# Optimization experiments

Hardware: AMD Instinct MI355X
Metric: run time of the kernel (lower is better)

Reference implementation:

```python
import jax, jax.numpy as jnp
import numpy as np

B, S, E = 2, 2048, 2048
NH, NKV, HD = 32, 8, 64
GS = NH // NKV  # group size = 4
EPS = 1e-6
ROPE_THETA = 10000.0


def setup_inputs() -> dict:
    key = jax.random.key(0)
    ks = jax.random.split(key, 6)
    x = jax.random.normal(ks[0], (B, S, E), jnp.float32)
    position_ids = jnp.broadcast_to(jnp.arange(S, dtype=jnp.int32), (B, S))
    # causal additive mask [1,1,S,S]
    causal = jnp.tril(jnp.ones((S, S), jnp.bool_))
    attn_mask = jnp.where(causal, 0.0, -1e9).astype(jnp.float32)[None, None]
    sc = 0.02
    Wq = jax.random.normal(ks[1], (E, NH * HD), jnp.float32) * sc
    Wk = jax.random.normal(ks[2], (E, NKV * HD), jnp.float32) * sc
    Wv = jax.random.normal(ks[3], (E, NKV * HD), jnp.float32) * sc
    Wo = jax.random.normal(ks[4], (NH * HD, E), jnp.float32) * sc
    q_norm_w = jnp.ones((HD,), jnp.float32)
    k_norm_w = jnp.ones((HD,), jnp.float32)
    return {"x": x, "position_ids": position_ids, "attn_mask": attn_mask,
            "Wq": Wq, "Wk": Wk, "Wv": Wv, "Wo": Wo,
            "q_norm_w": q_norm_w, "k_norm_w": k_norm_w}


def rms_norm(x, w):
    dt = x.dtype
    xf = x.astype(jnp.float32)
    xf = xf * jax.lax.rsqrt(jnp.mean(xf * xf, axis=-1, keepdims=True) + EPS)
    return w * xf.astype(dt)


def apply_rope(x, position_ids):
    # x: [B, H, S, D]; rotate-half RoPE
    D = x.shape[-1]
    inv_freq = 1.0 / (ROPE_THETA ** (jnp.arange(0, D, 2, dtype=jnp.float32) / D))
    freqs = position_ids.astype(jnp.float32)[:, :, None] * inv_freq  # [B,S,D/2]
    cos = jnp.cos(freqs)[:, None]  # [B,1,S,D/2]
    sin = jnp.sin(freqs)[:, None]
    x1, x2 = x[..., : D // 2], x[..., D // 2 :]
    return jnp.concatenate([x1 * cos - x2 * sin, x2 * cos + x1 * sin], axis=-1).astype(x.dtype)


def reference(x, position_ids, attn_mask, Wq, Wk, Wv, Wo, q_norm_w, k_norm_w):
    b, s, _ = x.shape
    Q = (x @ Wq).reshape(b, s, NH, HD).transpose(0, 2, 1, 3)   # [B,NH,S,D]
    K = (x @ Wk).reshape(b, s, NKV, HD).transpose(0, 2, 1, 3)  # [B,NKV,S,D]
    V = (x @ Wv).reshape(b, s, NKV, HD).transpose(0, 2, 1, 3)
    Q = rms_norm(Q, q_norm_w)
    K = rms_norm(K, k_norm_w)
    Q = apply_rope(Q, position_ids)
    K = apply_rope(K, position_ids)
    new_kv_cache = (K, V)
    # GQA: head h attends with kv group h // GS == reshape heads -> (NKV, GS)
    Qg = Q.reshape(b, NKV, GS, s, HD)
    scores = jnp.einsum('bgqsd,bgtd->bgqst', Qg, K) / np.float32(np.sqrt(HD))
    scores = scores + attn_mask[:, :, None]  # broadcast over group dim
    attn = jax.nn.softmax(scores.astype(jnp.float32), axis=-1).astype(x.dtype)
    ctx = jnp.einsum('bgqst,bgtd->bgqsd', attn, V)             # [B,NKV,GS,S,D]
    ctx = ctx.reshape(b, NH, s, HD).transpose(0, 2, 1, 3).reshape(b, s, NH * HD)
    output = ctx @ Wo
    return output, new_kv_cache
```

## Files before the change

kernel.cpp:

```cpp
#include <hip/hip_runtime.h>
#include <stdint.h>

#define S_LEN 2048
#define EMB 2048
#define NHEADS 32
#define NKVH 8
#define HDIM 64

typedef float f32x4 __attribute__((ext_vector_type(4)));
typedef float f32x16 __attribute__((ext_vector_type(16)));
typedef __bf16 bf16x8 __attribute__((ext_vector_type(8)));
typedef unsigned int u32x4 __attribute__((ext_vector_type(4)));

typedef const __attribute__((address_space(1))) void* as1cv;
typedef __attribute__((address_space(3))) void* as3v;

__device__ __forceinline__ void gload_lds16(const void* g, void* l) {
  as1cv gp = (as1cv)(uintptr_t)g;
  as3v lp = (as3v)(uintptr_t)l;
  __builtin_amdgcn_global_load_lds(gp, lp, 16, 0, 0);
}

__device__ __forceinline__ unsigned cvt_pk_bf16(float lo, float hi) {
  unsigned r;
// ... 71 lines not shown
  const int NT = K >> 6;
  const int nt = N / BN;
  const int nwg = (M / BM) * nt;
  const int q8 = nwg >> 3;
  int wg = blockIdx.x;
  int swz = (wg & 7) * q8 + (wg >> 3);
  int bm = swz / nt, bn = swz % nt;
  size_t m0 = (size_t)bm * BM, n0 = (size_t)bn * BN;

  int tid = threadIdx.x;
  int L = tid & 63, w = tid >> 6;
  int wrow = w >> 1, wcol = w & 1;
  int l15 = L & 15, hi2 = L >> 4;
  int lx = (l15 & 7) << 4;
  const int cx0 = (hi2 << 4) ^ lx;
  const int cx1 = (64 + (hi2 << 4)) ^ lx;

  int srow = tid >> 3;
  int scol = ((tid & 7) ^ (srow & 7)) << 3;
  const __bf16* pA = A + (size_t)(m0 + srow) * K + scol;
  const __bf16* pB = B + (size_t)(n0 + srow) * K + scol;

  char* smb = (char*)sm;
  const int aRow = (wrow * (BM / 2) + l15) * 128;
  const int bRow = (BM + wcol * (BN / 2) + l15) * 128;

  f32x4 acc[MF][NF];
#pragma unroll
  for (int m = 0; m < MF; ++m)
#pragma unroll
    for (int n = 0; n < NF; ++n) acc[m][n] = (f32x4){0.f, 0.f, 0.f, 0.f};

  auto STG = [&](int buf, int c, int t) {
    const __bf16* s = (c < CHA) ? pA + (size_t)(c << 5) * K + ((size_t)t << 6)
                                : pB + (size_t)((c - CHA) << 5) * K + ((size_t)t << 6);
    gload_lds16(s, smb + buf * (ROWS * 128) + c * 4096 + tid * 16);
  };

#pragma unroll
  for (int c = 0; c < NCALL; ++c) STG(0, c, 0);
#pragma unroll
  for (int c = 0; c < NCALL; ++c) STG(1, c, 1);
  if constexpr (NCALL == 10) asm volatile("s_waitcnt vmcnt(10)" ::: "memory");
  else asm volatile("s_waitcnt vmcnt(8)" ::: "memory");
  __builtin_amdgcn_s_barrier();

  for (int t = 0; t < NT; ++t) {
    const char* aC = smb + (t & 1) * (ROWS * 128);
    bf16x8 af[MF][2], bf[NF][2];
#pragma unroll
    for (int n = 0; n < NF; ++n) {
      bf[n][0] = *(const bf16x8*)(aC + bRow + n * 2048 + cx0);
      bf[n][1] = *(const bf16x8*)(aC + bRow + n * 2048 + cx1);
    }
#pragma unroll
    for (int m = 0; m < MF; ++m) {
      af[m][0] = *(const bf16x8*)(aC + aRow + m * 2048 + cx0);
      af[m][1] = *(const bf16x8*)(aC + aRow + m * 2048 + cx1);
    }
    asm volatile("s_waitcnt lgkmcnt(4)" ::: "memory");
    __builtin_amdgcn_sched_barrier(0);
    __builtin_amdgcn_s_setprio(1);
#pragma unroll
    for (int m = 0; m < MF / 2; ++m)
#pragma unroll
      for (int n = 0; n < NF; ++n)
#pragma unroll
        for (int kk = 0; kk < 2; ++kk)
          acc[m][n] = __builtin_amdgcn_mfma_f32_16x16x32_bf16(
              kk ? af[m][1] : af[m][0], kk ? bf[n][1] : bf[n][0], acc[m][n], 0, 0, 0);
    __builtin_amdgcn_s_setprio(0);
    asm volatile("s_waitcnt lgkmcnt(0)" ::: "memory");
    __builtin_amdgcn_sched_barrier(0);
    __builtin_amdgcn_s_barrier();
    if (t + 2 < NT) {
#pragma unroll
      for (int c = 0; c < NCALL; ++c) STG(t & 1, c, t + 2);
    }
    __builtin_amdgcn_s_setprio(1);
#pragma unroll
    for (int m = MF / 2; m < MF; ++m)
#pragma unroll
      for (int n = 0; n < NF; ++n)
#pragma unroll
        for (int kk = 0; kk < 2; ++kk)
          acc[m][n] = __builtin_amdgcn_mfma_f32_16x16x32_bf16(
              kk ? af[m][1] : af[m][0], kk ? bf[n][1] : bf[n][0], acc[m][n], 0, 0, 0);
    __builtin_amdgcn_s_setprio(0);
    if (t + 2 < NT) {
      if constexpr (NCALL == 10) asm volatile("s_waitcnt vmcnt(10)" ::: "memory");
      else asm volatile("s_waitcnt vmcnt(8)" ::: "memory");
    } else if (t + 1 < NT) {
      asm volatile("s_waitcnt vmcnt(0)" ::: "memory");
    }
    __builtin_amdgcn_s_barrier();
  }

#pragma unroll
  for (int m = 0; m < MF; ++m)
#pragma unroll
    for (int n = 0; n < NF; ++n)
#pragma unroll
      for (int r = 0; r < 4; ++r)
        C[(m0 + wrow * (BM / 2) + m * 16 + (hi2 << 2) + r) * (size_t)N + n0 +
          wcol * (BN / 2) + n * 16 + l15] = (OUT)acc[m][n][r];
}

__global__ __launch_bounds__(256) void rmsrope_kernel(
    const __bf16* __restrict__ QKV, const int* __restrict__ pos,
    const float* __restrict__ qw, const float* __restrict__ kw,
    const float* __restrict__ cosT, const float* __restrict__ sinT,
    __bf16* __restrict__ Qatt, __bf16* __restrict__ Katt, __bf16* __restrict__ Vtatt,
    float* __restrict__ Kc, float* __restrict__ Vc) {
  int token = blockIdx.x;
  int b = token >> 11, s = token & 2047;
  int tid = threadIdx.x, lane = tid & 63, wid = tid >> 6;
  int p = pos[token];
  int i = lane & 31;
  float cs = cosT[p * 32 + i], sn = sinT[p * 32 + i];
  const __bf16* base = QKV + (size_t)token * 3072;
  float qwl = qw[lane], kwl = kw[lane];
  const float qscale = 0.18033688011112042f;

  for (int h = wid; h < NHEADS; h += 4) {
    float v = (float)base[h * 64 + lane];
    float ss = v * v;
#pragma unroll
    for (int m = 1; m < 64; m <<= 1) ss += __shfl_xor(ss, m);
    float xn = v * rsqrtf(ss * (1.0f / 64.0f) + 1e-6f) * qwl;
    float other = __shfl_xor(xn, 32);
    float o = xn * cs + ((lane < 32) ? -other * sn : other * sn);
    Qatt[((size_t)(b * NHEADS + h) * S_LEN + s) * HDIM + lane] = (__bf16)(o * qscale);
  }
  for (int g = wid; g < NKVH; g += 4) {
    float v = (float)base[2048 + g * 64 + lane];
    float ss = v * v;
#pragma unroll
    for (int m = 1; m < 64; m <<= 1) ss += __shfl_xor(ss, m);
    float xn = v * rsqrtf(ss * (1.0f / 64.0f) + 1e-6f) * kwl;
    float other = __shfl_xor(xn, 32);
    float o = xn * cs + ((lane < 32) ? -other * sn : other * sn);
    size_t kidx = ((size_t)(b * NKVH + g) * S_LEN + s) * HDIM + lane;
    Katt[kidx] = (__bf16)o;
    Kc[kidx] = o;
  }
  for (int g = wid; g < NKVH; g += 4) {
    float v = (float)base[2560 + g * 64 + lane];
    size_t vidx = ((size_t)(b * NKVH + g) * S_LEN + s) * HDIM + lane;
    Vc[vidx] = v;
    Vtatt[((size_t)(b * NKVH + g) * HDIM + lane) * S_LEN + s] = (__bf16)v;
  }
}

__global__ __launch_bounds__(256, 2) void attn_kernel(const __bf16* __restrict__ Qatt,
                                                      const __bf16* __restrict__ Katt,
                                                      const __bf16* __restrict__ Vtatt,
                                                      __bf16* __restrict__ ctx) {
  __shared__ __align__(16) __bf16 Ks[2][4096];
  __shared__ __align__(16) __bf16 Vs[2][4096];
  int bid = blockIdx.x;
  int qt, bg;
  if (bid < 256) { qt = 31 - (bid >> 4); bg = bid & 15; }
  else { qt = (bid - 256) >> 4; bg = bid & 15; }
  int b = bg >> 3, g = bg & 7;
  int tid = threadIdx.x, lane = tid & 63, w = tid >> 6;
  int l31 = lane & 31, hi = lane >> 5;
  int h = g * 4 + w;

  const __bf16* Kg = Katt + (size_t)bg * (S_LEN * HDIM);
  const __bf16* Vg = Vtatt + (size_t)bg * (HDIM * S_LEN);
  const __bf16* Qg = Qatt + ((size_t)(b * NHEADS + h) * S_LEN + qt * 64 + l31) * HDIM;

  bf16x8 qf0[4], qf1[4];
#pragma unroll
  for (int ds = 0; ds < 4; ++ds) {
    qf0[ds] = *(const bf16x8*)(Qg + ds * 16 + (hi << 3));
    qf1[ds] = *(const bf16x8*)(Qg + 32 * HDIM + ds * 16 + (hi << 3));
  }

  f32x16 acc00, acc01, acc10, acc11;
#pragma unroll
  for (int r = 0; r < 16; ++r) { acc00[r] = 0.f; acc01[r] = 0.f; acc10[r] = 0.f; acc11[r] = 0.f; }
  float l0 = 0.f, l1 = 0.f;

  int sr = tid >> 3;
  int sc = ((tid & 7) ^ (sr & 7)) << 3;
  const __bf16* Ksrc = Kg + (size_t)sr * HDIM + sc;
  const __bf16* Vsrc = Vg + (size_t)sr * S_LEN + sc;

  gload_lds16(Ksrc, &Ks[0][tid * 8]);
  gload_lds16(Ksrc + 32 * HDIM, &Ks[0][2048 + tid * 8]);
  gload_lds16(Vsrc, &Vs[0][tid * 8]);
  gload_lds16(Vsrc + (size_t)32 * S_LEN, &Vs[0][2048 + tid * 8]);
  __syncthreads();

  int rx = (l31 & 7) << 4;

  for (int t = 0; t <= qt; ++t) {
    int cur = t & 1;
    if (t < qt) {
      const __bf16* kn = Ksrc + (size_t)(t + 1) * (64 * HDIM);
      const __bf16* vn = Vsrc + (size_t)(t + 1) * 64;
      gload_lds16(kn, &Ks[cur ^ 1][tid * 8]);
      gload_lds16(kn + 32 * HDIM, &Ks[cur ^ 1][2048 + tid * 8]);
      gload_lds16(vn, &Vs[cur ^ 1][tid * 8]);
      gload_lds16(vn + (size_t)32 * S_LEN, &Vs[cur ^ 1][2048 + tid * 8]);
    }
    f32x16 s00, s01, s10, s11;
#pragma unroll
    for (int r = 0; r < 16; ++r) { s00[r] = 0.f; s01[r] = 0.f; s10[r] = 0.f; s11[r] = 0.f; }
    {
      const char* kb0 = (const char*)Ks[cur] + (size_t)l31 * 128;
      const char* kb1 = kb0 + 4096;
#pragma unroll
      for (int dstep = 0; dstep < 4; ++dstep) {
        int cb = dstep * 32 + (hi << 4);
        bf16x8 k0 = *(const bf16x8*)(kb0 + (cb ^ rx));
        bf16x8 k1 = *(const bf16x8*)(kb1 + (cb ^ rx));
        s00 = __builtin_amdgcn_mfma_f32_32x32x16_bf16(k0, qf0[dstep], s00, 0, 0, 0);
        s01 = __builtin_amdgcn_mfma_f32_32x32x16_bf16(k1, qf0[dstep], s01, 0, 0, 0);
        s10 = __builtin_amdgcn_mfma_f32_32x32x16_bf16(k0, qf1[dstep], s10, 0, 0, 0);
        s11 = __builtin_amdgcn_mfma_f32_32x32x16_bf16(k1, qf1[dstep], s11, 0, 0, 0);
      }
    }
    if (t == qt) {
#pragma unroll
      for (int r = 0; r < 16; ++r) {
        int kb = (r & 3) + 8 * (r >> 2) + (hi << 2);
        if (kb > l31) { s00[r] = -3e38f; s11[r] = -3e38f; }
        s01[r] = -3e38f;
      }
    }
#pragma unroll
    for (int r = 0; r < 16; ++r) {
      s00[r] = __builtin_amdgcn_exp2f(s00[r]);
      s01[r] = __builtin_amdgcn_exp2f(s01[r]);
      s10[r] = __builtin_amdgcn_exp2f(s10[r]);
      s11[r] = __builtin_amdgcn_exp2f(s11[r]);
    }
    {
      float a0 = 0.f, a1 = 0.f, a2 = 0.f, a3 = 0.f;
      float b0 = 0.f, b1 = 0.f, b2 = 0.f, b3 = 0.f;
#pragma unroll
      for (int r = 0; r < 16; r += 4) {
        a0 += s00[r]; a1 += s00[r + 1]; a2 += s00[r + 2]; a3 += s00[r + 3];
        a0 += s01[r]; a1 += s01[r + 1]; a2 += s01[r + 2]; a3 += s01[r + 3];
        b0 += s10[r]; b1 += s10[r + 1]; b2 += s10[r + 2]; b3 += s10[r + 3];
        b0 += s11[r]; b1 += s11[r + 1]; b2 += s11[r + 2]; b3 += s11[r + 3];
      }
      l0 += (a0 + a1) + (a2 + a3);
      l1 += (b0 + b1) + (b2 + b3);
    }
    bf16x8 pf0[4], pf1[4];
    {
      unsigned wd[8];
#pragma unroll
      for (int i = 0; i < 8; ++i) wd[i] = cvt_pk_bf16(s00[2 * i], s00[2 * i + 1]);
      permswap(wd[0], wd[2]); permswap(wd[1], wd[3]);
      permswap(wd[4], wd[6]); permswap(wd[5], wd[7]);
      pf0[0] = pack4(wd[0], wd[1], wd[2], wd[3]);
      pf0[1] = pack4(wd[4], wd[5], wd[6], wd[7]);
#pragma unroll
      for (int i = 0; i < 8; ++i) wd[i] = cvt_pk_bf16(s01[2 * i], s01[2 * i + 1]);
      permswap(wd[0], wd[2]); permswap(wd[1], wd[3]);
      permswap(wd[4], wd[6]); permswap(wd[5], wd[7]);
      pf0[2] = pack4(wd[0], wd[1], wd[2], wd[3]);
      pf0[3] = pack4(wd[4], wd[5], wd[6], wd[7]);
#pragma unroll
      for (int i = 0; i < 8; ++i) wd[i] = cvt_pk_bf16(s10[2 * i], s10[2 * i + 1]);
      permswap(wd[0], wd[2]); permswap(wd[1], wd[3]);
      permswap(wd[4], wd[6]); permswap(wd[5], wd[7]);
      pf1[0] = pack4(wd[0], wd[1], wd[2], wd[3]);
      pf1[1] = pack4(wd[4], wd[5], wd[6], wd[7]);
#pragma unroll
      for (int i = 0; i < 8; ++i) wd[i] = cvt_pk_bf16(s11[2 * i], s11[2 * i + 1]);
      permswap(wd[0], wd[2]); permswap(wd[1], wd[3]);
      permswap(wd[4], wd[6]); permswap(wd[5], wd[7]);
      pf1[2] = pack4(wd[0], wd[1], wd[2], wd[3]);
      pf1[3] = pack4(wd[4], wd[5], wd[6], wd[7]);
    }
    {
      const char* vb0 = (const char*)Vs[cur] + (size_t)l31 * 128;
      const char* vb1 = vb0 + 4096;
#pragma unroll
      for (int ks = 0; ks < 4; ++ks) {
        int cb = ks * 32 + (hi << 4);
        bf16x8 v0 = *(const bf16x8*)(vb0 + (cb ^ rx));
        bf16x8 v1 = *(const bf16x8*)(vb1 + (cb ^ rx));
        acc00 = __builtin_amdgcn_mfma_f32_32x32x16_bf16(v0, pf0[ks], acc00, 0, 0, 0);
        acc01 = __builtin_amdgcn_mfma_f32_32x32x16_bf16(v1, pf0[ks], acc01, 0, 0, 0);
        acc10 = __builtin_amdgcn_mfma_f32_32x32x16_bf16(v0, pf1[ks], acc10, 0, 0, 0);
        acc11 = __builtin_amdgcn_mfma_f32_32x32x16_bf16(v1, pf1[ks], acc11, 0, 0, 0);
      }
    }
    __syncthreads();
  }

  l0 += __shfl_xor(l0, 32);
  l1 += __shfl_xor(l1, 32);
  float inv0 = 1.f / l0, inv1 = 1.f / l1;
  size_t orow0 = ((size_t)(b * S_LEN + qt * 64 + l31)) * EMB + h * HDIM;
  size_t orow1 = orow0 + (size_t)32 * EMB;
#pragma unroll
  for (int r = 0; r < 16; r += 2) {
    int d = (r & 3) + 8 * (r >> 2) + (hi << 2);
    unsigned w00 = cvt_pk_bf16(acc00[r] * inv0, acc00[r + 1] * inv0);
    unsigned w01 = cvt_pk_bf16(acc01[r] * inv0, acc01[r + 1] * inv0);
    unsigned w10 = cvt_pk_bf16(acc10[r] * inv1, acc10[r + 1] * inv1);
    unsigned w11 = cvt_pk_bf16(acc11[r] * inv1, acc11[r + 1] * inv1);
    *(unsigned*)((char*)ctx + (orow0 + d) * 2) = w00;
    *(unsigned*)((char*)ctx + (orow0 + 32 + d) * 2) = w01;
    *(unsigned*)((char*)ctx + (orow1 + d) * 2) = w10;
    *(unsigned*)((char*)ctx + (orow1 + 32 + d) * 2) = w11;
  }
}

extern "C" void kernel_launch(void* const* d_in, const int* in_sizes, int n_in,
                              void* d_out, int out_size, void* d_ws, size_t ws_size,
                              hipStream_t stream) {
  const float* x = (const float*)d_in[0];
  const int* pos = (const int*)d_in[1];
  const float* Wq = (const float*)d_in[3];
  const float* Wk = (const float*)d_in[4];
  const float* Wv = (const float*)d_in[5];
  const float* Wo = (const float*)d_in[6];
  const float* qw = (const float*)d_in[7];
  const float* kw = (const float*)d_in[8];

  float* out = (float*)d_out;
  float* Kc = out + (size_t)2 * 2048 * 2048;
  float* Vc = Kc + (size_t)2 * 8 * 2048 * 64;

  char* ws = (char*)d_ws;
  size_t off = 0;
  auto alloc = [&](size_t bytes) {
    char* p = ws + off;
    off += (bytes + 255) & ~(size_t)255;
    return (void*)p;
  };
  __bf16* xb = (__bf16*)alloc((size_t)4096 * 2048 * 2);
  __bf16* Wcat = (__bf16*)alloc((size_t)3072 * 2048 * 2);
  __bf16* Wot = (__bf16*)alloc((size_t)2048 * 2048 * 2);
  __bf16* QKV = (__bf16*)alloc((size_t)4096 * 3072 * 2);
  __bf16* ctx = (__bf16*)alloc((size_t)4096 * 2048 * 2);
  __bf16* Qatt = (__bf16*)alloc((size_t)2 * 32 * 2048 * 64 * 2);
  __bf16* Katt = (__bf16*)alloc((size_t)2 * 8 * 2048 * 64 * 2);
  __bf16* Vtat = (__bf16*)alloc((size_t)2 * 8 * 2048 * 64 * 2);
  float* cosT = (float*)alloc((size_t)2048 * 32 * 4);
  float* sinT = (float*)alloc((size_t)2048 * 32 * 4);

  rope_table_kernel<<<2048, 64, 0, stream>>>(cosT, sinT);
  cast_bf16_kernel<<<4096, 256, 0, stream>>>(x, xb, 4096 * 2048 / 8);
  transpose_cast_kernel<<<dim3(32, 32), 256, 0, stream>>>(Wq, Wcat, 2048, 2048);
  transpose_cast_kernel<<<dim3(8, 32), 256, 0, stream>>>(Wk, Wcat + (size_t)2048 * 2048, 2048, 512);
  transpose_cast_kernel<<<dim3(8, 32), 256, 0, stream>>>(Wv, Wcat + (size_t)2560 * 2048, 2048, 512);
  transpose_cast_kernel<<<dim3(32, 32), 256, 0, stream>>>(Wo, Wot, 2048, 2048);
  gemm4w_kernel<128, 192, __bf16><<<512, 256, 0, stream>>>(xb, Wcat, QKV, 4096, 3072, 2048);
  rmsrope_kernel<<<4096, 256, 0, stream>>>(QKV, pos, qw, kw, cosT, sinT, Qatt, Katt, Vtat, Kc, Vc);
  attn_kernel<<<512, 256, 0, stream>>>(Qatt, Katt, Vtat, ctx);
  gemm4w_kernel<128, 128, float><<<512, 256, 0, stream>>>(ctx, Wot, out, 4096, 2048, 2048);
}
```

Baseline: 186.2 us.

## Split KV tiles across two wave groups and pair causal q-tiles per block

The attention kernel now runs 512 threads per block. Two groups of four waves each process alternating KV tiles for the same query tile, and their partial accumulators and row sums are combined through LDS at the end. Each block handles both a long causal q-tile (31-x) and a short one (x) in sequence, which balances work across 256 blocks. Loads now stage two KV tiles at once with explicit waitcnt and barriers. This adds an LDS reduction and extra barriers, and drops occupancy to one block per CU in exchange for more in-flight work per query tile.

After: 188.2 us. About the same (+1.1%).

```diff
diff --git a/kernel.cpp b/kernel.cpp
--- a/kernel.cpp
+++ b/kernel.cpp
@@ -247,166 +247,216 @@
   }
 }
 
-__global__ __launch_bounds__(256, 2) void attn_kernel(const __bf16* __restrict__ Qatt,
+__global__ __launch_bounds__(512, 1) void attn_kernel(const __bf16* __restrict__ Qatt,
                                                       const __bf16* __restrict__ Katt,
                                                       const __bf16* __restrict__ Vtatt,
                                                       __bf16* __restrict__ ctx) {
-  __shared__ __align__(16) __bf16 Ks[2][4096];
-  __shared__ __align__(16) __bf16 Vs[2][4096];
+  __shared__ __align__(16) char smem[67584];
   int bid = blockIdx.x;
-  int qt, bg;
-  if (bid < 256) { qt = 31 - (bid >> 4); bg = bid & 15; }
-  else { qt = (bid - 256) >> 4; bg = bid & 15; }
+  int x = bid >> 4;
+  int bg = bid & 15;
   int b = bg >> 3, g = bg & 7;
   int tid = threadIdx.x, lane = tid & 63, w = tid >> 6;
+  int hq = w & 3, par = w >> 2;
+  int h = g * 4 + hq;
   int l31 = lane & 31, hi = lane >> 5;
-  int h = g * 4 + w;
+  int rx = (l31 & 7) << 4;
 
   const __bf16* Kg = Katt + (size_t)bg * (S_LEN * HDIM);
   const __bf16* Vg = Vtatt + (size_t)bg * (HDIM * S_LEN);
-  const __bf16* Qg = Qatt + ((size_t)(b * NHEADS + h) * S_LEN + qt * 64 + l31) * HDIM;
-
-  bf16x8 qf0[4], qf1[4];
-#pragma unroll
-  for (int ds = 0; ds < 4; ++ds) {
-    qf0[ds] = *(const bf16x8*)(Qg + ds * 16 + (hi << 3));
-    qf1[ds] = *(const bf16x8*)(Qg + 32 * HDIM + ds * 16 + (hi << 3));
-  }
-
-  f32x16 acc00, acc01, acc10, acc11;
-#pragma unroll
-  for (int r = 0; r < 16; ++r) { acc00[r] = 0.f; acc01[r] = 0.f; acc10[r] = 0.f; acc11[r] = 0.f; }
-  float l0 = 0.f, l1 = 0.f;
 
   int sr = tid >> 3;
   int sc = ((tid & 7) ^ (sr & 7)) << 3;
   const __bf16* Ksrc = Kg + (size_t)sr * HDIM + sc;
   const __bf16* Vsrc = Vg + (size_t)sr * S_LEN + sc;
 
-  gload_lds16(Ksrc, &Ks[0][tid * 8]);
-  gload_lds16(Ksrc + 32 * HDIM, &Ks[0][2048 + tid * 8]);
-  gload_lds16(Vsrc, &Vs[0][tid * 8]);
-  gload_lds16(Vsrc + (size_t)32 * S_LEN, &Vs[0][2048 + tid * 8]);
-  __syncthreads();
-
-  int rx = (l31 & 7) << 4;
-
-  for (int t = 0; t <= qt; ++t) {
-    int cur = t & 1;
-    if (t < qt) {
-      const __bf16* kn = Ksrc + (size_t)(t + 1) * (64 * HDIM);
-      const __bf16* vn = Vsrc + (size_t)(t + 1) * 64;
-      gload_lds16(kn, &Ks[cur ^ 1][tid * 8]);
-      gload_lds16(kn + 32 * HDIM, &Ks[cur ^ 1][2048 + tid * 8]);
-      gload_lds16(vn, &Vs[cur ^ 1][tid * 8]);
-      gload_lds16(vn + (size_t)32 * S_LEN, &Vs[cur ^ 1][2048 + tid * 8]);
-    }
-    f32x16 s00, s01, s10, s11;
-#pragma unroll
-    for (int r = 0; r < 16; ++r) { s00[r] = 0.f; s01[r] = 0.f; s10[r] = 0.f; s11[r] = 0.f; }
-    {
-      const char* kb0 = (const char*)Ks[cur] + (size_t)l31 * 128;
-      const char* kb1 = kb0 + 4096;
-#pragma unroll
-      for (int dstep = 0; dstep < 4; ++dstep) {
-        int cb = dstep * 32 + (hi << 4);
-        bf16x8 k0 = *(const bf16x8*)(kb0 + (cb ^ rx));
-        bf16x8 k1 = *(const bf16x8*)(kb1 + (cb ^ rx));
-        s00 = __builtin_amdgcn_mfma_f32_32x32x16_bf16(k0, qf0[dstep], s00, 0, 0, 0);
-        s01 = __builtin_amdgcn_mfma_f32_32x32x16_bf16(k1, qf0[dstep], s01, 0, 0, 0);
-        s10 = __builtin_amdgcn_mfma_f32_32x32x16_bf16(k0, qf1[dstep], s10, 0, 0, 0);
-        s11 = __builtin_amdgcn_mfma_f32_32x32x16_bf16(k1, qf1[dstep], s11, 0, 0, 0);
+  float* lm = (float*)(smem + 65536);
+
+  auto STAGE = [&](int pair, int slot, int t) {
+    gload_lds16(Ksrc + (size_t)t * (64 * HDIM), smem + (pair * 2 + slot) * 8192 + tid * 16);
+    gload_lds16(Vsrc + (size_t)t * 64, smem + 32768 + (pair * 2 + slot) * 8192 + tid * 16);
+  };
+
+#pragma unroll 1
+  for (int phase = 0; phase < 2; ++phase) {
+    int qt = phase == 0 ? (31 - x) : x;
+    const __bf16* Qg = Qatt + ((size_t)(b * NHEADS + h) * S_LEN + qt * 64 + l31) * HDIM;
+    bf16x8 qf0[4], qf1[4];
+#pragma unroll
+    for (int ds = 0; ds < 4; ++ds) {
+      qf0[ds] = *(const bf16x8*)(Qg + ds * 16 + (hi << 3));
+      qf1[ds] = *(const bf16x8*)(Qg + 32 * HDIM + ds * 16 + (hi << 3));
+    }
+    f32x16 acc00, acc01, acc10, acc11;
+#pragma unroll
+    for (int r = 0; r < 16; ++r) { acc00[r] = 0.f; acc01[r] = 0.f; acc10[r] = 0.f; acc11[r] = 0.f; }
+    float l0 = 0.f, l1 = 0.f;
+
+    int niter = (qt + 2) >> 1;
+    STAGE(0, 0, 0);
+    STAGE(0, 1, qt > 0 ? 1 : 0);
+
+#pragma unroll 1
+    for (int i = 0; i < niter; ++i) {
+      int pcur = i & 1;
+      int ta = 2 * i + 2;
+      if (ta <= qt) {
+        int tb = (ta + 1 <= qt) ? ta + 1 : qt;
+        STAGE(pcur ^ 1, 0, ta);
+        STAGE(pcur ^ 1, 1, tb);
+        asm volatile("s_waitcnt vmcnt(4)" ::: "memory");
+      } else {
+        asm volatile("s_waitcnt vmcnt(0)" ::: "memory");
       }
-    }
-    if (t == qt) {
-#pragma unroll
-      for (int r = 0; r < 16; ++r) {
-        int kb = (r & 3) + 8 * (r >> 2) + (hi << 2);
-        if (kb > l31) { s00[r] = -3e38f; s11[r] = -3e38f; }
-        s01[r] = -3e38f;
+      __builtin_amdgcn_s_barrier();
+      int t = 2 * i + par;
+      if (t <= qt) {
+        const char* Kt = smem + (pcur * 2 + par) * 8192;
+        const char* Vt = smem + 32768 + (pcur * 2 + par) * 8192;
+        f32x16 s00, s01, s10, s11;
+#pragma unroll
+        for (int r = 0; r < 16; ++r) { s00[r] = 0.f; s01[r] = 0.f; s10[r] = 0.f; s11[r] = 0.f; }
+        {
+          const char* kb0 = Kt + (size_t)l31 * 128;
+          const char* kb1 = kb0 + 4096;
+#pragma unroll
+          for (int dstep = 0; dstep < 4; ++dstep) {
+            int cb = dstep * 32 + (hi << 4);
+            bf16x8 k0 = *(const bf16x8*)(kb0 + (cb ^ rx));
+            bf16x8 k1 = *(const bf16x8*)(kb1 + (cb ^ rx));
+            s00 = __builtin_amdgcn_mfma_f32_32x32x16_bf16(k0, qf0[dstep], s00, 0, 0, 0);
+            s01 = __builtin_amdgcn_mfma_f32_32x32x16_bf16(k1, qf0[dstep], s01, 0, 0, 0);
+            s10 = __builtin_amdgcn_mfma_f32_32x32x16_bf16(k0, qf1[dstep], s10, 0, 0, 0);
+            s11 = __builtin_amdgcn_mfma_f32_32x32x16_bf16(k1, qf1[dstep], s11, 0, 0, 0);
+          }
+        }
+        if (t == qt) {
+#pragma unroll
+          for (int r = 0; r < 16; ++r) {
+            int kb = (r & 3) + 8 * (r >> 2) + (hi << 2);
+            if (kb > l31) { s00[r] = -3e38f; s11[r] = -3e38f; }
+            s01[r] = -3e38f;
+          }
+        }
+#pragma unroll
+        for (int r = 0; r < 16; ++r) {
+          s00[r] = __builtin_amdgcn_exp2f(s00[r]);
+          s01[r] = __builtin_amdgcn_exp2f(s01[r]);
+          s10[r] = __builtin_amdgcn_exp2f(s10[r]);
+          s11[r] = __builtin_amdgcn_exp2f(s11[r]);
+        }
+        {
+          float a0 = 0.f, a1 = 0.f, a2 = 0.f, a3 = 0.f;
+          float b0 = 0.f, b1 = 0.f, b2 = 0.f, b3 = 0.f;
+#pragma unroll
+          for (int r = 0; r < 16; r += 4) {
+            a0 += s00[r]; a1 += s00[r + 1]; a2 += s00[r + 2]; a3 += s00[r + 3];
+            a0 += s01[r]; a1 += s01[r + 1]; a2 += s01[r + 2]; a3 += s01[r + 3];
+            b0 += s10[r]; b1 += s10[r + 1]; b2 += s10[r + 2]; b3 += s10[r + 3];
+            b0 += s11[r]; b1 += s11[r + 1]; b2 += s11[r + 2]; b3 += s11[r + 3];
+          }
+          l0 += (a0 + a1) + (a2 + a3);
+          l1 += (b0 + b1) + (b2 + b3);
+        }
+        bf16x8 pf0[4], pf1[4];
+        {
+          unsigned wd[8];
+#pragma unroll
+          for (int j = 0; j < 8; ++j) wd[j] = cvt_pk_bf16(s00[2 * j], s00[2 * j + 1]);
+          permswap(wd[0], wd[2]); permswap(wd[1], wd[3]);
+          permswap(wd[4], wd[6]); permswap(wd[5], wd[7]);
+          pf0[0] = pack4(wd[0], wd[1], wd[2], wd[3]);
+          pf0[1] = pack4(wd[4], wd[5], wd[6], wd[7]);
+#pragma unroll
+          for (int j = 0; j < 8; ++j) wd[j] = cvt_pk_bf16(s01[2 * j], s01[2 * j + 1]);
+          permswap(wd[0], wd[2]); permswap(wd[1], wd[3]);
+          permswap(wd[4], wd[6]); permswap(wd[5], wd[7]);
+          pf0[2] = pack4(wd[0], wd[1], wd[2], wd[3]);
+          pf0[3] = pack4(wd[4], wd[5], wd[6], wd[7]);
+#pragma unroll
+          for (int j = 0; j < 8; ++j) wd[j] = cvt_pk_bf16(s10[2 * j], s10[2 * j + 1]);
+          permswap(wd[0], wd[2]); permswap(wd[1], wd[3]);
+          permswap(wd[4], wd[6]); permswap(wd[5], wd[7]);
+          pf1[0] = pack4(wd[0], wd[1], wd[2], wd[3]);
+          pf1[1] = pack4(wd[4], wd[5], wd[6], wd[7]);
+#pragma unroll
+          for (int j = 0; j < 8; ++j) wd[j] = cvt_pk_bf16(s11[2 * j], s11[2 * j + 1]);
+          permswap(wd[0], wd[2]); permswap(wd[1], wd[3]);
+          permswap(wd[4], wd[6]); permswap(wd[5], wd[7]);
+          pf1[2] = pack4(wd[0], wd[1], wd[2], wd[3]);
+          pf1[3] = pack4(wd[4], wd[5], wd[6], wd[7]);
+        }
+        {
+          const char* vb0 = Vt + (size_t)l31 * 128;
+          const char* vb1 = vb0 + 4096;
+#pragma unroll
+          for (int ks = 0; ks < 4; ++ks) {
+            int cb = ks * 32 + (hi << 4);
+            bf16x8 v0 = *(const bf16x8*)(vb0 + (cb ^ rx));
+            bf16x8 v1 = *(const bf16x8*)(vb1 + (cb ^ rx));
+            acc00 = __builtin_amdgcn_mfma_f32_32x32x16_bf16(v0, pf0[ks], acc00, 0, 0, 0);
+            acc01 = __builtin_amdgcn_mfma_f32_32x32x16_bf16(v1, pf0[ks], acc01, 0, 0, 0);
+            acc10 = __builtin_amdgcn_mfma_f32_32x32x16_bf16(v0, pf1[ks], acc10, 0, 0, 0);
+            acc11 = __builtin_amdgcn_mfma_f32_32x32x16_bf16(v1, pf1[ks], acc11, 0, 0, 0);
+          }
+        }
       }
-    }
-#pragma unroll
-    for (int r = 0; r < 16; ++r) {
-      s00[r] = __builtin_amdgcn_exp2f(s00[r]);
-      s01[r] = __builtin_amdgcn_exp2f(s01[r]);
-      s10[r] = __builtin_amdgcn_exp2f(s10[r]);
-      s11[r] = __builtin_amdgcn_exp2f(s11[r]);
-    }
-    {
-      float a0 = 0.f, a1 = 0.f, a2 = 0.f, a3 = 0.f;
-      float b0 = 0.f, b1 = 0.f, b2 = 0.f, b3 = 0.f;
-#pragma unroll
-      for (int r = 0; r < 16; r += 4) {
-        a0 += s00[r]; a1 += s00[r + 1]; a2 += s00[r + 2]; a3 += s00[r + 3];
-        a0 += s01[r]; a1 += s01[r + 1]; a2 += s01[r + 2]; a3 += s01[r + 3];
-        b0 += s10[r]; b1 += s10[r + 1]; b2 += s10[r + 2]; b3 += s10[r + 3];
-        b0 += s11[r]; b1 += s11[r + 1]; b2 += s11[r + 2]; b3 += s11[r + 3];
+      asm volatile("s_waitcnt lgkmcnt(0)" ::: "memory");
+      __builtin_amdgcn_sched_barrier(0);
+      __builtin_amdgcn_s_barrier();
+    }
+
+    char* om = smem + hq * 16384 + lane * 16;
+    if (par == 1) {
+#pragma unroll
+      for (int j = 0; j < 4; ++j) {
+        *(f32x4*)(om + j * 1024) = (f32x4){acc00[4 * j], acc00[4 * j + 1], acc00[4 * j + 2], acc00[4 * j + 3]};
+        *(f32x4*)(om + (4 + j) * 1024) = (f32x4){acc01[4 * j], acc01[4 * j + 1], acc01[4 * j + 2], acc01[4 * j + 3]};
+        *(f32x4*)(om + (8 + j) * 1024) = (f32x4){acc10[4 * j], acc10[4 * j + 1], acc10[4 * j + 2], acc10[4 * j + 3]};
+        *(f32x4*)(om + (12 + j) * 1024) = (f32x4){acc11[4 * j], acc11[4 * j + 1], acc11[4 * j + 2], acc11[4 * j + 3]};
       }
-      l0 += (a0 + a1) + (a2 + a3);
-      l1 += (b0 + b1) + (b2 + b3);
-    }
-    bf16x8 pf0[4], pf1[4];
-    {
-      unsigned wd[8];
-#pragma unroll
-      for (int i = 0; i < 8; ++i) wd[i] = cvt_pk_bf16(s00[2 * i], s00[2 * i + 1]);
-      permswap(wd[0], wd[2]); permswap(wd[1], wd[3]);
-      permswap(wd[4], wd[6]); permswap(wd[5], wd[7]);
-      pf0[0] = pack4(wd[0], wd[1], wd[2], wd[3]);
-      pf0[1] = pack4(wd[4], wd[5], wd[6], wd[7]);
-#pragma unroll
-      for (int i = 0; i < 8; ++i) wd[i] = cvt_pk_bf16(s01[2 * i], s01[2 * i + 1]);
-      permswap(wd[0], wd[2]); permswap(wd[1], wd[3]);
-      permswap(wd[4], wd[6]); permswap(wd[5], wd[7]);
-      pf0[2] = pack4(wd[0], wd[1], wd[2], wd[3]);
-      pf0[3] = pack4(wd[4], wd[5], wd[6], wd[7]);
-#pragma unroll
-      for (int i = 0; i < 8; ++i) wd[i] = cvt_pk_bf16(s10[2 * i], s10[2 * i + 1]);
-      permswap(wd[0], wd[2]); permswap(wd[1], wd[3]);
-      permswap(wd[4], wd[6]); permswap(wd[5], wd[7]);
-      pf1[0] = pack4(wd[0], wd[1], wd[2], wd[3]);
-      pf1[1] = pack4(wd[4], wd[5], wd[6], wd[7]);
-#pragma unroll
-      for (int i = 0; i < 8; ++i) wd[i] = cvt_pk_bf16(s11[2 * i], s11[2 * i + 1]);
-      permswap(wd[0], wd[2]); permswap(wd[1], wd[3]);
-      permswap(wd[4], wd[6]); permswap(wd[5], wd[7]);
-      pf1[2] = pack4(wd[0], wd[1], wd[2], wd[3]);
-      pf1[3] = pack4(wd[4], wd[5], wd[6], wd[7]);
-    }
-    {
-      const char* vb0 = (const char*)Vs[cur] + (size_t)l31 * 128;
-      const char* vb1 = vb0 + 4096;
-#pragma unroll
-      for (int ks = 0; ks < 4; ++ks) {
-        int cb = ks * 32 + (hi << 4);
-        bf16x8 v0 = *(const bf16x8*)(vb0 + (cb ^ rx));
-        bf16x8 v1 = *(const bf16x8*)(vb1 + (cb ^ rx));
-        acc00 = __builtin_amdgcn_mfma_f32_32x32x16_bf16(v0, pf0[ks], acc00, 0, 0, 0);
-        acc01 = __builtin_amdgcn_mfma_f32_32x32x16_bf16(v1, pf0[ks], acc01, 0, 0, 0);
-        acc10 = __builtin_amdgcn_mfma_f32_32x32x16_bf16(v0, pf1[ks], acc10, 0, 0, 0);
-        acc11 = __builtin_amdgcn_mfma_f32_32x32x16_bf16(v1, pf1[ks], acc11, 0, 0, 0);
+      lm[hq * 128 + lane] = l0;
+      lm[hq * 128 + 64 + lane] = l1;
+    }
+    asm volatile("s_waitcnt lgkmcnt(0)" ::: "memory");
+    __builtin_amdgcn_s_barrier();
+    if (par == 0) {
+#pragma unroll
+      for (int j = 0; j < 4; ++j) {
+        f32x4 c0 = *(const f32x4*)(om + j * 1024);
+        f32x4 c1 = *(const f32x4*)(om + (4 + j) * 1024);
+        f32x4 c2 = *(const f32x4*)(om + (8 + j) * 1024);
+        f32x4 c3 = *(const f32x4*)(om + (12 + j) * 1024);
+#pragma unroll
+        for (int e = 0; e < 4; ++e) {
+          acc00[4 * j + e] += c0[e];
+          acc01[4 * j + e] += c1[e];
+          acc10[4 * j + e] += c2[e];
+          acc11[4 * j + e] += c3[e];
+        }
       }
-    }
-    __syncthreads();
-  }
-
-  l0 += __shfl_xor(l0, 32);
-  l1 += __shfl_xor(l1, 32);
-  float inv0 = 1.f / l0, inv1 = 1.f / l1;
-  size_t orow0 = ((size_t)(b * S_LEN + qt * 64 + l31)) * EMB + h * HDIM;
-  size_t orow1 = orow0 + (size_t)32 * EMB;
-#pragma unroll
-  for (int r = 0; r < 16; r += 2) {
-    int d = (r & 3) + 8 * (r >> 2) + (hi << 2);
-    unsigned w00 = cvt_pk_bf16(acc00[r] * inv0, acc00[r + 1] * inv0);
-    unsigned w01 = cvt_pk_bf16(acc01[r] * inv0, acc01[r + 1] * inv0);
-    unsigned w10 = cvt_pk_bf16(acc10[r] * inv1, acc10[r + 1] * inv1);
-    unsigned w11 = cvt_pk_bf16(acc11[r] * inv1, acc11[r + 1] * inv1);
-    *(unsigned*)((char*)ctx + (orow0 + d) * 2) = w00;
-    *(unsigned*)((char*)ctx + (orow0 + 32 + d) * 2) = w01;
-    *(unsigned*)((char*)ctx + (orow1 + d) * 2) = w10;
-    *(unsigned*)((char*)ctx + (orow1 + 32 + d) * 2) = w11;
+      l0 += lm[hq * 128 + lane];
+      l1 += lm[hq * 128 + 64 + lane];
+      l0 += __shfl_xor(l0, 32);
+      l1 += __shfl_xor(l1, 32);
+      float inv0 = 1.f / l0, inv1 = 1.f / l1;
+      size_t orow0 = ((size_t)(b * S_LEN + qt * 64 + l31)) * EMB + h * HDIM;
+      size_t orow1 = orow0 + (size_t)32 * EMB;
+#pragma unroll
+      for (int r = 0; r < 16; r += 2) {
+        int d = (r & 3) + 8 * (r >> 2) + (hi << 2);
+        unsigned w00 = cvt_pk_bf16(acc00[r] * inv0, acc00[r + 1] * inv0);
+        unsigned w01 = cvt_pk_bf16(acc01[r] * inv0, acc01[r + 1] * inv0);
+        unsigned w10 = cvt_pk_bf16(acc10[r] * inv1, acc10[r + 1] * inv1);
+        unsigned w11 = cvt_pk_bf16(acc11[r] * inv1, acc11[r + 1] * inv1);
+        *(unsigned*)((char*)ctx + (orow0 + d) * 2) = w00;
+        *(unsigned*)((char*)ctx + (orow0 + 32 + d) * 2) = w01;
+        *(unsigned*)((char*)ctx + (orow1 + d) * 2) = w10;
+        *(unsigned*)((char*)ctx + (orow1 + 32 + d) * 2) = w11;
+      }
+    }
+    asm volatile("s_waitcnt lgkmcnt(0)" ::: "memory");
+    __builtin_amdgcn_s_barrier();
   }
 }
 
@@ -452,6 +502,6 @@
   transpose_cast_kernel<<<dim3(32, 32), 256, 0, stream>>>(Wo, Wot, 2048, 2048);
   gemm4w_kernel<128, 192, __bf16><<<512, 256, 0, stream>>>(xb, Wcat, QKV, 4096, 3072, 2048);
   rmsrope_kernel<<<4096, 256, 0, stream>>>(QKV, pos, qw, kw, cosT, sinT, Qatt, Katt, Vtat, Kc, Vc);
-  attn_kernel<<<512, 256, 0, stream>>>(Qatt, Katt, Vtat, ctx);
+  attn_kernel<<<256, 512, 0, stream>>>(Qatt, Katt, Vtat, ctx);
   gemm4w_kernel<128, 128, float><<<512, 256, 0, stream>>>(ctx, Wot, out, 4096, 2048, 2048);
 }
```

## Pair complementary 32-row query tiles per block with triple-buffered K/V staging

Applied to the files above, without the earlier changes.

The attention kernel now gives each warp 32 query rows instead of 64. Each block processes two complementary causal tiles (j and 63-j) one after the other, so every block does an equal amount of work. K/V tiles are staged through a three-slot LDS ring with explicit vmcnt waits, which lets loads run two tiles ahead, and the MFMA sections are raised with s_setprio. The cost is that each K/V tile loaded into LDS now serves half as many query rows, which raises LDS read traffic per MFMA and adds barrier overhead.

After: 192.6 us. 1.03x slower.

```diff
diff --git a/kernel.cpp b/kernel.cpp
--- a/kernel.cpp
+++ b/kernel.cpp
@@ -251,162 +251,153 @@
                                                       const __bf16* __restrict__ Katt,
                                                       const __bf16* __restrict__ Vtatt,
                                                       __bf16* __restrict__ ctx) {
-  __shared__ __align__(16) __bf16 Ks[2][4096];
-  __shared__ __align__(16) __bf16 Vs[2][4096];
+  __shared__ __align__(16) char smem[49152];
   int bid = blockIdx.x;
-  int qt, bg;
-  if (bid < 256) { qt = 31 - (bid >> 4); bg = bid & 15; }
-  else { qt = (bid - 256) >> 4; bg = bid & 15; }
+  int p = bid >> 4, bg = bid & 15;
   int b = bg >> 3, g = bg & 7;
   int tid = threadIdx.x, lane = tid & 63, w = tid >> 6;
   int l31 = lane & 31, hi = lane >> 5;
   int h = g * 4 + w;
+  int rx = (l31 & 7) << 4;
 
   const __bf16* Kg = Katt + (size_t)bg * (S_LEN * HDIM);
   const __bf16* Vg = Vtatt + (size_t)bg * (HDIM * S_LEN);
-  const __bf16* Qg = Qatt + ((size_t)(b * NHEADS + h) * S_LEN + qt * 64 + l31) * HDIM;
-
-  bf16x8 qf0[4], qf1[4];
-#pragma unroll
-  for (int ds = 0; ds < 4; ++ds) {
-    qf0[ds] = *(const bf16x8*)(Qg + ds * 16 + (hi << 3));
-    qf1[ds] = *(const bf16x8*)(Qg + 32 * HDIM + ds * 16 + (hi << 3));
-  }
-
-  f32x16 acc00, acc01, acc10, acc11;
-#pragma unroll
-  for (int r = 0; r < 16; ++r) { acc00[r] = 0.f; acc01[r] = 0.f; acc10[r] = 0.f; acc11[r] = 0.f; }
-  float l0 = 0.f, l1 = 0.f;
 
   int sr = tid >> 3;
   int sc = ((tid & 7) ^ (sr & 7)) << 3;
   const __bf16* Ksrc = Kg + (size_t)sr * HDIM + sc;
   const __bf16* Vsrc = Vg + (size_t)sr * S_LEN + sc;
 
-  gload_lds16(Ksrc, &Ks[0][tid * 8]);
-  gload_lds16(Ksrc + 32 * HDIM, &Ks[0][2048 + tid * 8]);
-  gload_lds16(Vsrc, &Vs[0][tid * 8]);
-  gload_lds16(Vsrc + (size_t)32 * S_LEN, &Vs[0][2048 + tid * 8]);
-  __syncthreads();
-
-  int rx = (l31 & 7) << 4;
-
-  for (int t = 0; t <= qt; ++t) {
-    int cur = t & 1;
-    if (t < qt) {
-      const __bf16* kn = Ksrc + (size_t)(t + 1) * (64 * HDIM);
-      const __bf16* vn = Vsrc + (size_t)(t + 1) * 64;
-      gload_lds16(kn, &Ks[cur ^ 1][tid * 8]);
-      gload_lds16(kn + 32 * HDIM, &Ks[cur ^ 1][2048 + tid * 8]);
-      gload_lds16(vn, &Vs[cur ^ 1][tid * 8]);
-      gload_lds16(vn + (size_t)32 * S_LEN, &Vs[cur ^ 1][2048 + tid * 8]);
-    }
-    f32x16 s00, s01, s10, s11;
-#pragma unroll
-    for (int r = 0; r < 16; ++r) { s00[r] = 0.f; s01[r] = 0.f; s10[r] = 0.f; s11[r] = 0.f; }
-    {
-      const char* kb0 = (const char*)Ks[cur] + (size_t)l31 * 128;
-      const char* kb1 = kb0 + 4096;
-#pragma unroll
-      for (int dstep = 0; dstep < 4; ++dstep) {
-        int cb = dstep * 32 + (hi << 4);
-        bf16x8 k0 = *(const bf16x8*)(kb0 + (cb ^ rx));
-        bf16x8 k1 = *(const bf16x8*)(kb1 + (cb ^ rx));
-        s00 = __builtin_amdgcn_mfma_f32_32x32x16_bf16(k0, qf0[dstep], s00, 0, 0, 0);
-        s01 = __builtin_amdgcn_mfma_f32_32x32x16_bf16(k1, qf0[dstep], s01, 0, 0, 0);
-        s10 = __builtin_amdgcn_mfma_f32_32x32x16_bf16(k0, qf1[dstep], s10, 0, 0, 0);
-        s11 = __builtin_amdgcn_mfma_f32_32x32x16_bf16(k1, qf1[dstep], s11, 0, 0, 0);
-      }
-    }
-    if (t == qt) {
+  auto STAGE = [&](int slot, int t) {
+    char* base = smem + slot * 16384;
+    const __bf16* kt = Ksrc + (size_t)t * (64 * HDIM);
+    const __bf16* vt = Vsrc + (size_t)t * 64;
+    gload_lds16(kt, base + tid * 16);
+    gload_lds16(kt + 32 * HDIM, base + 4096 + tid * 16);
+    gload_lds16(vt, base + 8192 + tid * 16);
+    gload_lds16(vt + (size_t)32 * S_LEN, base + 12288 + tid * 16);
+  };
+
+#pragma unroll 1
+  for (int phase = 0; phase < 2; ++phase) {
+    int j = phase ? (63 - p) : p;
+    int tl = j >> 1;
+    const __bf16* Qg = Qatt + ((size_t)(b * NHEADS + h) * S_LEN + j * 32 + l31) * HDIM;
+    bf16x8 qf[4];
+#pragma unroll
+    for (int ds = 0; ds < 4; ++ds) qf[ds] = *(const bf16x8*)(Qg + ds * 16 + (hi << 3));
+
+    f32x16 acc0, acc1;
+#pragma unroll
+    for (int r = 0; r < 16; ++r) { acc0[r] = 0.f; acc1[r] = 0.f; }
+    float l_run = 0.f;
+
+    STAGE(0, 0);
+    if (tl >= 1) STAGE(1, 1);
+
+#pragma unroll 1
+    for (int i = 0; i <= tl; ++i) {
+      if (i + 2 <= tl) {
+        STAGE((i + 2) % 3, i + 2);
+        asm volatile("s_waitcnt vmcnt(8)" ::: "memory");
+      } else if (i + 1 <= tl) {
+        asm volatile("s_waitcnt vmcnt(4)" ::: "memory");
+      } else {
+        asm volatile("s_waitcnt vmcnt(0)" ::: "memory");
+      }
+      __builtin_amdgcn_s_barrier();
+
+      const char* Kt = smem + (i % 3) * 16384;
+      const char* Vt = Kt + 8192;
+      f32x16 s0, s1;
+#pragma unroll
+      for (int r = 0; r < 16; ++r) { s0[r] = 0.f; s1[r] = 0.f; }
+      {
+        const char* kb0 = Kt + (size_t)l31 * 128;
+        const char* kb1 = kb0 + 4096;
+        __builtin_amdgcn_s_setprio(1);
+#pragma unroll
+        for (int dstep = 0; dstep < 4; ++dstep) {
+          int cb = dstep * 32 + (hi << 4);
+          bf16x8 k0 = *(const bf16x8*)(kb0 + (cb ^ rx));
+          bf16x8 k1 = *(const bf16x8*)(kb1 + (cb ^ rx));
+          s0 = __builtin_amdgcn_mfma_f32_32x32x16_bf16(k0, qf[dstep], s0, 0, 0, 0);
+          s1 = __builtin_amdgcn_mfma_f32_32x32x16_bf16(k1, qf[dstep], s1, 0, 0, 0);
+        }
+        __builtin_amdgcn_s_setprio(0);
+      }
+      if (i == tl) {
+#pragma unroll
+        for (int r = 0; r < 16; ++r) {
+          int kb = (r & 3) + 8 * (r >> 2) + (hi << 2);
+          if (j & 1) {
+            if (kb > l31) s1[r] = -3e38f;
+          } else {
+            if (kb > l31) s0[r] = -3e38f;
+            s1[r] = -3e38f;
+          }
+        }
+      }
 #pragma unroll
       for (int r = 0; r < 16; ++r) {
-        int kb = (r & 3) + 8 * (r >> 2) + (hi << 2);
-        if (kb > l31) { s00[r] = -3e38f; s11[r] = -3e38f; }
-        s01[r] = -3e38f;
-      }
-    }
-#pragma unroll
-    for (int r = 0; r < 16; ++r) {
-      s00[r] = __builtin_amdgcn_exp2f(s00[r]);
-      s01[r] = __builtin_amdgcn_exp2f(s01[r]);
-      s10[r] = __builtin_amdgcn_exp2f(s10[r]);
-      s11[r] = __builtin_amdgcn_exp2f(s11[r]);
-    }
-    {
-      float a0 = 0.f, a1 = 0.f, a2 = 0.f, a3 = 0.f;
-      float b0 = 0.f, b1 = 0.f, b2 = 0.f, b3 = 0.f;
-#pragma unroll
-      for (int r = 0; r < 16; r += 4) {
-        a0 += s00[r]; a1 += s00[r + 1]; a2 += s00[r + 2]; a3 += s00[r + 3];
-        a0 += s01[r]; a1 += s01[r + 1]; a2 += s01[r + 2]; a3 += s01[r + 3];
-        b0 += s10[r]; b1 += s10[r + 1]; b2 += s10[r + 2]; b3 += s10[r + 3];
-        b0 += s11[r]; b1 += s11[r + 1]; b2 += s11[r + 2]; b3 += s11[r + 3];
-      }
-      l0 += (a0 + a1) + (a2 + a3);
-      l1 += (b0 + b1) + (b2 + b3);
-    }
-    bf16x8 pf0[4], pf1[4];
-    {
-      unsigned wd[8];
-#pragma unroll
-      for (int i = 0; i < 8; ++i) wd[i] = cvt_pk_bf16(s00[2 * i], s00[2 * i + 1]);
-      permswap(wd[0], wd[2]); permswap(wd[1], wd[3]);
-      permswap(wd[4], wd[6]); permswap(wd[5], wd[7]);
-      pf0[0] = pack4(wd[0], wd[1], wd[2], wd[3]);
-      pf0[1] = pack4(wd[4], wd[5], wd[6], wd[7]);
-#pragma unroll
-      for (int i = 0; i < 8; ++i) wd[i] = cvt_pk_bf16(s01[2 * i], s01[2 * i + 1]);
-      permswap(wd[0], wd[2]); permswap(wd[1], wd[3]);
-      permswap(wd[4], wd[6]); permswap(wd[5], wd[7]);
-      pf0[2] = pack4(wd[0], wd[1], wd[2], wd[3]);
-      pf0[3] = pack4(wd[4], wd[5], wd[6], wd[7]);
-#pragma unroll
-      for (int i = 0; i < 8; ++i) wd[i] = cvt_pk_bf16(s10[2 * i], s10[2 * i + 1]);
-      permswap(wd[0], wd[2]); permswap(wd[1], wd[3]);
-      permswap(wd[4], wd[6]); permswap(wd[5], wd[7]);
-      pf1[0] = pack4(wd[0], wd[1], wd[2], wd[3]);
-      pf1[1] = pack4(wd[4], wd[5], wd[6], wd[7]);
-#pragma unroll
-      for (int i = 0; i < 8; ++i) wd[i] = cvt_pk_bf16(s11[2 * i], s11[2 * i + 1]);
-      permswap(wd[0], wd[2]); permswap(wd[1], wd[3]);
-      permswap(wd[4], wd[6]); permswap(wd[5], wd[7]);
-      pf1[2] = pack4(wd[0], wd[1], wd[2], wd[3]);
-      pf1[3] = pack4(wd[4], wd[5], wd[6], wd[7]);
-    }
-    {
-      const char* vb0 = (const char*)Vs[cur] + (size_t)l31 * 128;
-      const char* vb1 = vb0 + 4096;
-#pragma unroll
-      for (int ks = 0; ks < 4; ++ks) {
-        int cb = ks * 32 + (hi << 4);
-        bf16x8 v0 = *(const bf16x8*)(vb0 + (cb ^ rx));
-        bf16x8 v1 = *(const bf16x8*)(vb1 + (cb ^ rx));
-        acc00 = __builtin_amdgcn_mfma_f32_32x32x16_bf16(v0, pf0[ks], acc00, 0, 0, 0);
-        acc01 = __builtin_amdgcn_mfma_f32_32x32x16_bf16(v1, pf0[ks], acc01, 0, 0, 0);
-        acc10 = __builtin_amdgcn_mfma_f32_32x32x16_bf16(v0, pf1[ks], acc10, 0, 0, 0);
-        acc11 = __builtin_amdgcn_mfma_f32_32x32x16_bf16(v1, pf1[ks], acc11, 0, 0, 0);
-      }
-    }
-    __syncthreads();
-  }
-
-  l0 += __shfl_xor(l0, 32);
-  l1 += __shfl_xor(l1, 32);
-  float inv0 = 1.f / l0, inv1 = 1.f / l1;
-  size_t orow0 = ((size_t)(b * S_LEN + qt * 64 + l31)) * EMB + h * HDIM;
-  size_t orow1 = orow0 + (size_t)32 * EMB;
-#pragma unroll
-  for (int r = 0; r < 16; r += 2) {
-    int d = (r & 3) + 8 * (r >> 2) + (hi << 2);
-    unsigned w00 = cvt_pk_bf16(acc00[r] * inv0, acc00[r + 1] * inv0);
-    unsigned w01 = cvt_pk_bf16(acc01[r] * inv0, acc01[r + 1] * inv0);
-    unsigned w10 = cvt_pk_bf16(acc10[r] * inv1, acc10[r + 1] * inv1);
-    unsigned w11 = cvt_pk_bf16(acc11[r] * inv1, acc11[r + 1] * inv1);
-    *(unsigned*)((char*)ctx + (orow0 + d) * 2) = w00;
-    *(unsigned*)((char*)ctx + (orow0 + 32 + d) * 2) = w01;
-    *(unsigned*)((char*)ctx + (orow1 + d) * 2) = w10;
-    *(unsigned*)((char*)ctx + (orow1 + 32 + d) * 2) = w11;
+        s0[r] = __builtin_amdgcn_exp2f(s0[r]);
+        s1[r] = __builtin_amdgcn_exp2f(s1[r]);
+      }
+      {
+        float a0 = 0.f, a1 = 0.f, a2 = 0.f, a3 = 0.f;
+#pragma unroll
+        for (int r = 0; r < 16; r += 4) {
+          a0 += s0[r]; a1 += s0[r + 1]; a2 += s0[r + 2]; a3 += s0[r + 3];
+          a0 += s1[r]; a1 += s1[r + 1]; a2 += s1[r + 2]; a3 += s1[r + 3];
+        }
+        l_run += (a0 + a1) + (a2 + a3);
+      }
+      bf16x8 pf[4];
+      {
+        unsigned wd[8];
+#pragma unroll
+        for (int q = 0; q < 8; ++q) wd[q] = cvt_pk_bf16(s0[2 * q], s0[2 * q + 1]);
+        permswap(wd[0], wd[2]); permswap(wd[1], wd[3]);
+        permswap(wd[4], wd[6]); permswap(wd[5], wd[7]);
+        pf[0] = pack4(wd[0], wd[1], wd[2], wd[3]);
+        pf[1] = pack4(wd[4], wd[5], wd[6], wd[7]);
+#pragma unroll
+        for (int q = 0; q < 8; ++q) wd[q] = cvt_pk_bf16(s1[2 * q], s1[2 * q + 1]);
+        permswap(wd[0], wd[2]); permswap(wd[1], wd[3]);
+        permswap(wd[4], wd[6]); permswap(wd[5], wd[7]);
+        pf[2] = pack4(wd[0], wd[1], wd[2], wd[3]);
+        pf[3] = pack4(wd[4], wd[5], wd[6], wd[7]);
+      }
+      {
+        const char* vb0 = Vt + (size_t)l31 * 128;
+        const char* vb1 = vb0 + 4096;
+        __builtin_amdgcn_s_setprio(1);
+#pragma unroll
+        for (int ks = 0; ks < 4; ++ks) {
+          int cb = ks * 32 + (hi << 4);
+          bf16x8 v0 = *(const bf16x8*)(vb0 + (cb ^ rx));
+          bf16x8 v1 = *(const bf16x8*)(vb1 + (cb ^ rx));
+          acc0 = __builtin_amdgcn_mfma_f32_32x32x16_bf16(v0, pf[ks], acc0, 0, 0, 0);
+          acc1 = __builtin_amdgcn_mfma_f32_32x32x16_bf16(v1, pf[ks], acc1, 0, 0, 0);
+        }
+        __builtin_amdgcn_s_setprio(0);
+      }
+      asm volatile("s_waitcnt lgkmcnt(0)" ::: "memory");
+      __builtin_amdgcn_sched_barrier(0);
+      __builtin_amdgcn_s_barrier();
+    }
+
+    l_run += __shfl_xor(l_run, 32);
+    float inv = 1.f / l_run;
+    size_t orow = ((size_t)(b * S_LEN + j * 32 + l31)) * EMB + h * HDIM;
+#pragma unroll
+    for (int r = 0; r < 16; r += 2) {
+      int d = (r & 3) + 8 * (r >> 2) + (hi << 2);
+      unsigned w0 = cvt_pk_bf16(acc0[r] * inv, acc0[r + 1] * inv);
+      unsigned w1 = cvt_pk_bf16(acc1[r] * inv, acc1[r + 1] * inv);
+      *(unsigned*)((char*)ctx + (orow + d) * 2) = w0;
+      *(unsigned*)((char*)ctx + (orow + 32 + d) * 2) = w1;
+    }
   }
 }
 
```

## Triple-buffer K/V tiles in attention with explicit vmcnt waits and MFMA priority

Applied to the files above, without the earlier changes.

Replaces the double-buffered K/V LDS staging with a three-slot ring that prefetches two tiles ahead. Explicit s_waitcnt vmcnt counts let the kernel wait only for the current tile's loads, with raw s_barrier in place of __syncthreads. The MFMA sections are wrapped in s_setprio to favour matrix issue across waves. LDS use grows from 32KB to 48KB per block, which may limit how many blocks fit per CU, and the hand-set vmcnt values depend on the exact number of outstanding loads.

New measurement: 190.5 us. +2.3%, slower.

```diff
diff --git a/kernel.cpp b/kernel.cpp
--- a/kernel.cpp
+++ b/kernel.cpp
@@ -251,8 +251,7 @@
                                                       const __bf16* __restrict__ Katt,
                                                       const __bf16* __restrict__ Vtatt,
                                                       __bf16* __restrict__ ctx) {
-  __shared__ __align__(16) __bf16 Ks[2][4096];
-  __shared__ __align__(16) __bf16 Vs[2][4096];
+  __shared__ __align__(16) char smem[49152];
   int bid = blockIdx.x;
   int qt, bg;
   if (bid < 256) { qt = 31 - (bid >> 4); bg = bid & 15; }
@@ -261,6 +260,7 @@
   int tid = threadIdx.x, lane = tid & 63, w = tid >> 6;
   int l31 = lane & 31, hi = lane >> 5;
   int h = g * 4 + w;
+  int rx = (l31 & 7) << 4;
 
   const __bf16* Kg = Katt + (size_t)bg * (S_LEN * HDIM);
   const __bf16* Vg = Vtatt + (size_t)bg * (HDIM * S_LEN);
@@ -283,30 +283,40 @@
   const __bf16* Ksrc = Kg + (size_t)sr * HDIM + sc;
   const __bf16* Vsrc = Vg + (size_t)sr * S_LEN + sc;
 
-  gload_lds16(Ksrc, &Ks[0][tid * 8]);
-  gload_lds16(Ksrc + 32 * HDIM, &Ks[0][2048 + tid * 8]);
-  gload_lds16(Vsrc, &Vs[0][tid * 8]);
-  gload_lds16(Vsrc + (size_t)32 * S_LEN, &Vs[0][2048 + tid * 8]);
-  __syncthreads();
-
-  int rx = (l31 & 7) << 4;
-
+  auto STAGE = [&](int slot, int t) {
+    char* base = smem + slot * 16384;
+    const __bf16* kt = Ksrc + (size_t)t * (64 * HDIM);
+    const __bf16* vt = Vsrc + (size_t)t * 64;
+    gload_lds16(kt, base + tid * 16);
+    gload_lds16(kt + 32 * HDIM, base + 4096 + tid * 16);
+    gload_lds16(vt, base + 8192 + tid * 16);
+    gload_lds16(vt + (size_t)32 * S_LEN, base + 12288 + tid * 16);
+  };
+
+  STAGE(0, 0);
+  if (qt >= 1) STAGE(1, 1);
+
+#pragma unroll 1
   for (int t = 0; t <= qt; ++t) {
-    int cur = t & 1;
-    if (t < qt) {
-      const __bf16* kn = Ksrc + (size_t)(t + 1) * (64 * HDIM);
-      const __bf16* vn = Vsrc + (size_t)(t + 1) * 64;
-      gload_lds16(kn, &Ks[cur ^ 1][tid * 8]);
-      gload_lds16(kn + 32 * HDIM, &Ks[cur ^ 1][2048 + tid * 8]);
-      gload_lds16(vn, &Vs[cur ^ 1][tid * 8]);
-      gload_lds16(vn + (size_t)32 * S_LEN, &Vs[cur ^ 1][2048 + tid * 8]);
-    }
+    if (t + 2 <= qt) {
+      STAGE((t + 2) % 3, t + 2);
+      asm volatile("s_waitcnt vmcnt(8)" ::: "memory");
+    } else if (t + 1 <= qt) {
+      asm volatile("s_waitcnt vmcnt(4)" ::: "memory");
+    } else {
+      asm volatile("s_waitcnt vmcnt(0)" ::: "memory");
+    }
+    __builtin_amdgcn_s_barrier();
+
+    const char* Kt = smem + (t % 3) * 16384;
+    const char* Vt = Kt + 8192;
     f32x16 s00, s01, s10, s11;
 #pragma unroll
     for (int r = 0; r < 16; ++r) { s00[r] = 0.f; s01[r] = 0.f; s10[r] = 0.f; s11[r] = 0.f; }
     {
-      const char* kb0 = (const char*)Ks[cur] + (size_t)l31 * 128;
+      const char* kb0 = Kt + (size_t)l31 * 128;
       const char* kb1 = kb0 + 4096;
+      __builtin_amdgcn_s_setprio(1);
 #pragma unroll
       for (int dstep = 0; dstep < 4; ++dstep) {
         int cb = dstep * 32 + (hi << 4);
@@ -317,6 +327,7 @@
         s10 = __builtin_amdgcn_mfma_f32_32x32x16_bf16(k0, qf1[dstep], s10, 0, 0, 0);
         s11 = __builtin_amdgcn_mfma_f32_32x32x16_bf16(k1, qf1[dstep], s11, 0, 0, 0);
       }
+      __builtin_amdgcn_s_setprio(0);
     }
     if (t == qt) {
 #pragma unroll
@@ -375,8 +386,9 @@
       pf1[3] = pack4(wd[4], wd[5], wd[6], wd[7]);
     }
     {
-      const char* vb0 = (const char*)Vs[cur] + (size_t)l31 * 128;
+      const char* vb0 = Vt + (size_t)l31 * 128;
       const char* vb1 = vb0 + 4096;
+      __builtin_amdgcn_s_setprio(1);
 #pragma unroll
       for (int ks = 0; ks < 4; ++ks) {
         int cb = ks * 32 + (hi << 4);
@@ -387,8 +399,11 @@
         acc10 = __builtin_amdgcn_mfma_f32_32x32x16_bf16(v0, pf1[ks], acc10, 0, 0, 0);
         acc11 = __builtin_amdgcn_mfma_f32_32x32x16_bf16(v1, pf1[ks], acc11, 0, 0, 0);
       }
-    }
-    __syncthreads();
+      __builtin_amdgcn_s_setprio(0);
+    }
+    asm volatile("s_waitcnt lgkmcnt(0)" ::: "memory");
+    __builtin_amdgcn_sched_barrier(0);
+    __builtin_amdgcn_s_barrier();
   }
 
   l0 += __shfl_xor(l0, 32);
```
